# Kernel tuning notes

Measured on AMD Instinct MI355X. Metric: run time of the kernel, lower is better.

Reference implementation:

```python
import jax, jax.numpy as jnp
import numpy as np

B, S, C, H = 2, 3144, 256, 8
HD = C // H                      # head_dim = key_dim = 32
SCALE = HD ** -0.5
QN = 8                           # queriesNum hard-coded in source
KS = 5                           # lepe depthwise conv kernel


def setup_inputs() -> dict:
    key = jax.random.key(0)
    ks = jax.random.split(key, 10)
    gain_qkv = 2 ** (-2.5) * (2.0 / (C + C)) ** 0.5  # xavier_normal std with gain 2^-2.5
    gain_out = (2.0 / (C + C)) ** 0.5
    return {
        "x": jax.random.normal(ks[0], (B, S, C), jnp.float32),
        "mask": jax.random.uniform(ks[1], (B, S, S), jnp.float32),
        "wq": jax.random.normal(ks[2], (C, C), jnp.float32) * gain_qkv,
        "bq": jnp.zeros((C,), jnp.float32),
        "wk": jax.random.normal(ks[3], (C, C), jnp.float32) * gain_qkv,
        "bk": jnp.zeros((C,), jnp.float32),
        "wv": jax.random.normal(ks[4], (C, C), jnp.float32) * gain_qkv,
        "bv": jnp.zeros((C,), jnp.float32),
        "lepe_w": jax.random.normal(ks[5], (KS, KS, 1, C), jnp.float32) * 0.05,  # depthwise HWIO
        "lepe_b": jnp.zeros((C,), jnp.float32),
        "wo": jax.random.normal(ks[6], (C, C), jnp.float32) * gain_out,
        "bo": jnp.zeros((C,), jnp.float32),
        "h": 56,
        "w": 56,
    }


def _dwconv(x_nhwc, kern, bias):
    # depthwise 5x5, stride 1, padding 2 (groups = channels)
    y = jax.lax.conv_general_dilated(
        x_nhwc, kern, window_strides=(1, 1), padding=((2, 2), (2, 2)),
        dimension_numbers=("NHWC", "HWIO", "NHWC"),
        feature_group_count=x_nhwc.shape[-1])
    return y + bias


def reference(x, mask, wq, bq, wk, bk, wv, bv, lepe_w, lepe_b, wo, bo, h, w):
    b, s, c = x.shape
    q = x @ wq.T + bq
    k = (x @ wk.T + bk) * SCALE
    v = x @ wv.T + bv
    # lepe positional residual on the non-query tokens
    lepe = _dwconv(v[:, QN:].reshape(b, h, w, c), lepe_w, lepe_b).reshape(b, h * w, c)
    qh = q.reshape(b, s, H, HD).transpose(0, 2, 1, 3)   # (b, H, s, hd)
    kh = k.reshape(b, s, H, HD).transpose(0, 2, 1, 3)
    vh = kh  # faithful to source: v_h = k.reshape(...)  (scaled k used as values)
    qk = jnp.einsum("bhqd,bhkd->bhqk", qh, kh)
    qk = qk + jnp.log(mask[:, None] + 1e-6)              # isSoftMask=True path
    attn = jax.nn.softmax(qk, axis=-1)
    out = jnp.einsum("bhqk,bhkd->bhqd", attn, vh)
    out = out.transpose(0, 2, 1, 3).reshape(b, s, c)
    out = out.at[:, QN:].add(lepe)
    return out @ wo.T + bo
```

## Files before the change

### kernel.cpp

```cpp
#include <hip/hip_runtime.h>


#define S_LEN 3144
#define SP    3200
#define HEADS 8
#define HD    32
#define BATCH 2
#define MROWS (BATCH*S_LEN)
#define NPIX  3136
#define SCALE_F 0.17677669529663687f
#define KQ_SC   0.25504472665352026f

typedef __bf16 bf16x8  __attribute__((ext_vector_type(8)));
typedef __bf16 bf16x4  __attribute__((ext_vector_type(4)));
typedef float  floatx4 __attribute__((ext_vector_type(4)));
typedef short  shortx4 __attribute__((ext_vector_type(4)));
typedef _Float16 halfx4 __attribute__((ext_vector_type(4)));
typedef _Float16 halfx8 __attribute__((ext_vector_type(8)));

static __device__ __forceinline__ float bf2f(unsigned int h) {
  union { unsigned int u; float f; } v; v.u = h << 16; return v.f;
}
static __device__ __forceinline__ unsigned short f2bf(float f) {
  union { __bf16 b; unsigned short u; } v; v.b = (__bf16)f; return v.u;
}
static __device__ __forceinline__ bf16x8 ldcvt8(const float* __restrict__ p) {
  float4 a = *(const float4*)p;
  float4 b = *(const float4*)(p + 4);
  bf16x8 r;
  r[0]=(__bf16)a.x; r[1]=(__bf16)a.y; r[2]=(__bf16)a.z; r[3]=(__bf16)a.w;
  r[4]=(__bf16)b.x; r[5]=(__bf16)b.y; r[6]=(__bf16)b.z; r[7]=(__bf16)b.w;
  return r;
}

#define GLOBAL_AS __attribute__((address_space(1)))
#define LDS_AS    __attribute__((address_space(3)))
static __device__ __forceinline__ void gload_lds16(const void* g, void* l) {
  __builtin_amdgcn_global_load_lds((const GLOBAL_AS void*)g, (LDS_AS void*)l, 16, 0, 0);
}

#define FENCE4() asm volatile("s_waitcnt vmcnt(4)" ::: "memory")
#define FENCE2() asm volatile("s_waitcnt vmcnt(2)" ::: "memory")
#define FENCE0() asm volatile("s_waitcnt vmcnt(0)" ::: "memory")

__global__ __launch_bounds__(256) void k_prep(
    const float* __restrict__ x, const float* __restrict__ wq,
    const float* __restrict__ wk, const float* __restrict__ wv,
    unsigned short* __restrict__ xb, unsigned short* __restrict__ w3b,
    const float* __restrict__ mask, _Float16* __restrict__ pm)
{
  const int blk = blockIdx.x;
  if (blk < 882) {
    const int i = blk * 256 + threadIdx.x;
    const int NX = MROWS * 32;
    const int NW = 8192;
    const float* src;
    unsigned short* dst;
    if (i < NX) { src = x + (size_t)i * 8; dst = xb + (size_t)i * 8; }
    else {
      const int j = i - NX;
      if (j >= 3 * NW) return;
      src = (j < NW) ? wq + (size_t)j * 8
          : (j < 2 * NW) ? wk + (size_t)(j - NW) * 8
                         : wv + (size_t)(j - 2 * NW) * 8;
      dst = w3b + (size_t)j * 8;
    }
    bf16x8 v = ldcvt8(src);
    *(bf16x8*)dst = v;
    return;
  }
  const int mp = blk - 882;
  const int bs = mp % 400;
  const int by = mp / 400;
  const int b  = bs / 200, strip = bs % 200;
  const int t  = threadIdx.x;
  const int n  = t & 127;
  const int tsel = t >> 7;
  const int row = n >> 3;
  const int k2  = n & 7;
  const int g0  = (2 * k2) ^ (row & 15);
  const int gbase = g0 & ~1;
  const bool swp = (g0 & 1);

  int mr = strip * 16 + row; if (mr >= S_LEN) mr = S_LEN - 1;
  const float* src = mask + ((size_t)b * S_LEN + mr) * S_LEN;
  _Float16* dst0 = pm + ((size_t)bs * 50) * 1024 + n * 8;

#pragma unroll 1
  for (int tt = 0; tt < 5; ++tt) {
    const int tile = by * 10 + tt * 2 + tsel;
    const int c0 = tile * 64 + gbase * 4;
    float4 a = make_float4(-1e-6f, -1e-6f, -1e-6f, -1e-6f);
    float4 c = a;
    if (c0 < S_LEN) {
      a = *(const float4*)(src + c0);
      c = *(const float4*)(src + c0 + 4);
    }
    const float4 fst = swp ? c : a;
    const float4 snd = swp ? a : c;
    halfx8 o;
    o[0] = (_Float16)(fst.x + 1e-6f); o[1] = (_Float16)(fst.y + 1e-6f);
    o[2] = (_Float16)(fst.z + 1e-6f); o[3] = (_Float16)(fst.w + 1e-6f);
    o[4] = (_Float16)(snd.x + 1e-6f); o[5] = (_Float16)(snd.y + 1e-6f);
    o[6] = (_Float16)(snd.z + 1e-6f); o[7] = (_Float16)(snd.w + 1e-6f);
    *(halfx8*)(dst0 + (size_t)tile * 1024) = o;
  }
}

__global__ __launch_bounds__(256) void k_qkv(
    const unsigned short* __restrict__ xb, const unsigned short* __restrict__ w3b,
    const float* __restrict__ bqp, const float* __restrict__ bkp,
    const float* __restrict__ bvp,
    unsigned short* __restrict__ qws, unsigned short* __restrict__ kws,
    unsigned short* __restrict__ vfrag, unsigned short* __restrict__ vstage)
{
  __shared__ unsigned short lds_t[64 * 65];
  const int lane = threadIdx.x & 63;
  const int wid  = threadIdx.x >> 6;
  const int c    = lane & 15, quad = lane >> 4;
  const int bsel  = blockIdx.x / 50;
  const int stile = blockIdx.x % 50;
  const int srow0 = stile * 64;
  const int ncol = blockIdx.y * 64;
  const int wsel = ncol >> 8;
  const int col0 = ncol & 255;

  const float* bptr = (wsel == 0) ? bqp : (wsel == 1) ? bkp : bvp;

  const int srow = srow0 + wid * 16 + c;
  const int arow = bsel * S_LEN + ((srow < S_LEN) ? srow : 0);
  const unsigned short* ap = xb  + (size_t)arow * 256 + quad * 8;
  const unsigned short* bp = w3b + (size_t)(ncol + c) * 256 + quad * 8;

  floatx4 acc[4];
#pragma unroll
  for (int ct = 0; ct < 4; ++ct) acc[ct] = (floatx4){0.f, 0.f, 0.f, 0.f};

#pragma unroll
  for (int ks = 0; ks < 8; ++ks) {
    bf16x8 af = *(const bf16x8*)(ap + ks * 32);
#pragma unroll
    for (int ct = 0; ct < 4; ++ct) {
      bf16x8 bf = *(const bf16x8*)(bp + (size_t)ct * 16 * 256 + ks * 32);
      acc[ct] = __builtin_amdgcn_mfma_f32_16x16x32_bf16(af, bf, acc[ct], 0, 0, 0);
    }
  }

#pragma unroll
  for (int ct = 0; ct < 4; ++ct) {
    const int col = col0 + ct * 16 + c;
    const float bias = bptr[col];
#pragma unroll
    for (int r = 0; r < 4; ++r) {
      const int s = srow0 + wid * 16 + quad * 4 + r;
      const int valid = (s < S_LEN);
      const float v = acc[ct][r] + bias;
      if (wsel == 0) {
        qws[(((size_t)(bsel * HEADS + (col >> 5))) * SP + s) * HD + (col & 31)] =
            valid ? f2bf(v) : (unsigned short)0;
      } else if (wsel == 1) {
        kws[(((size_t)(bsel * HEADS + (col >> 5))) * SP + s) * HD + (col & 31)] =
            valid ? f2bf(v * KQ_SC) : (unsigned short)0;
        lds_t[(ct * 16 + c) * 65 + (wid * 16 + quad * 4 + r)] =
            valid ? f2bf(v * SCALE_F) : (unsigned short)0;
      } else {
        if (valid) vstage[(size_t)(bsel * S_LEN + s) * 256 + col] = f2bf(v);
      }
    }
  }

  if (wsel == 1) {
    __syncthreads();
    const int tid = threadIdx.x;
#pragma unroll
    for (int j = 0; j < 4; ++j) {
      const int grp  = j * 4 + (tid >> 6);
      const int l    = tid & 63;
      const int ct2  = grp & 3;
      const int half = (grp >> 2) & 1;
      const int hsel = grp >> 3;
      const int cc = l & 15, qq = l >> 4;
      const int cl = hsel * 32 + half * 16 + cc;
      const int rb = ct2 * 16 + qq * 4;
      union { shortx4 s4; unsigned short u[4]; } pk;
#pragma unroll
      for (int e = 0; e < 4; ++e) pk.u[e] = lds_t[cl * 65 + rb + e];
      const int hglob = (col0 >> 5) + hsel;
      const size_t off =
          ((((size_t)(bsel * HEADS + hglob) * 50 + stile) * 4 + ct2) * 2 + half) * 64 + l;
      *(shortx4*)(vfrag + off * 4) = pk.s4;
    }
  }
}

__global__ __launch_bounds__(256) void k_lepe(const unsigned short* __restrict__ vws,
                                              const float* __restrict__ cw,
                                              const float* __restrict__ cb,
                                              unsigned short* __restrict__ lepe)
{
  int idx = blockIdx.x * 256 + threadIdx.x;
  if (idx >= BATCH * NPIX * 32) return;
  const int cg = idx & 31;
  const int p  = (idx >> 5) % NPIX;
  const int b  = idx / (NPIX * 32);
  const int y  = p / 56, xx = p - y * 56;

  float acc[8];
  {
    float4 b0 = *(const float4*)(cb + cg * 8);
    float4 b1 = *(const float4*)(cb + cg * 8 + 4);
    acc[0]=b0.x; acc[1]=b0.y; acc[2]=b0.z; acc[3]=b0.w;
    acc[4]=b1.x; acc[5]=b1.y; acc[6]=b1.z; acc[7]=b1.w;
  }
#pragma unroll
  for (int dy = -2; dy <= 2; ++dy) {
    const int yy = y + dy;
    if ((unsigned)yy >= 56u) continue;
#pragma unroll
    for (int dx = -2; dx <= 2; ++dx) {
      const int xs = xx + dx;
      if ((unsigned)xs >= 56u) continue;
      uint4 vv = *(const uint4*)(vws + (size_t)(b * S_LEN + 8 + yy * 56 + xs) * 256 + cg * 8);
      const float* wp = cw + (size_t)((dy + 2) * 5 + (dx + 2)) * 256 + cg * 8;
      float4 w0 = *(const float4*)wp;
      float4 w1 = *(const float4*)(wp + 4);
      unsigned int va[4] = {vv.x, vv.y, vv.z, vv.w};
      acc[0] += bf2f(va[0] & 0xFFFFu) * w0.x;  acc[1] += bf2f(va[0] >> 16) * w0.y;
      acc[2] += bf2f(va[1] & 0xFFFFu) * w0.z;  acc[3] += bf2f(va[1] >> 16) * w0.w;
      acc[4] += bf2f(va[2] & 0xFFFFu) * w1.x;  acc[5] += bf2f(va[2] >> 16) * w1.y;
      acc[6] += bf2f(va[3] & 0xFFFFu) * w1.z;  acc[7] += bf2f(va[3] >> 16) * w1.w;
    }
  }
  unsigned int o[4];
#pragma unroll
  for (int j = 0; j < 4; ++j)
    o[j] = (unsigned int)f2bf(acc[2*j]) | ((unsigned int)f2bf(acc[2*j+1]) << 16);
  *((uint4*)(lepe + (size_t)(b * NPIX + p) * 256 + cg * 8)) = make_uint4(o[0], o[1], o[2], o[3]);
}

static __device__ __forceinline__ void proc_tile_pre(
    int t, const unsigned short* __restrict__ kb,
    const unsigned short* __restrict__ vb,
    const _Float16* __restrict__ mb,
    int c, int quad, int lane, const bf16x8 qf,
    floatx4& o0, floatx4& o1, float& l_run)
{
  const int k0 = t * 64;
  bf16x8 kf[4]; shortx4 v0[4], v1[4];
  const unsigned short* tb = vb + (size_t)t * 2048;
#pragma unroll
  for (int ct = 0; ct < 4; ++ct) {
    kf[ct] = *(const bf16x8*)(kb + (size_t)(k0 + ct * 16 + c) * HD + quad * 8);
    v0[ct] = *(const shortx4*)(tb + (ct * 2 + 0) * 256 + lane * 4);
    v1[ct] = *(const shortx4*)(tb + (ct * 2 + 1) * 256 + lane * 4);
  }
  floatx4 s[4];
#pragma unroll
  for (int ct = 0; ct < 4; ++ct)
    s[ct] = __builtin_amdgcn_mfma_f32_16x16x32_bf16(kf[ct], qf,
               (floatx4){0.f,0.f,0.f,0.f}, 0, 0, 0);
  float ls = 0.f;
  shortx4 pf[4];
#pragma unroll
  for (int ct = 0; ct < 4; ++ct) {
    const halfx4 mv = *(const halfx4*)(mb + c * 64 + (((ct * 4 + quad) ^ c) * 4));
    float pr[4];
    pr[0] = (float)mv[0] * __builtin_amdgcn_exp2f(s[ct][0]);
    pr[1] = (float)mv[1] * __builtin_amdgcn_exp2f(s[ct][1]);
    pr[2] = (float)mv[2] * __builtin_amdgcn_exp2f(s[ct][2]);
    pr[3] = (float)mv[3] * __builtin_amdgcn_exp2f(s[ct][3]);
    ls += (pr[0] + pr[1]) + (pr[2] + pr[3]);
    union { bf16x4 b4; shortx4 s4; } u;
    u.b4[0]=(__bf16)pr[0]; u.b4[1]=(__bf16)pr[1]; u.b4[2]=(__bf16)pr[2]; u.b4[3]=(__bf16)pr[3];
    pf[ct] = u.s4;
  }
  l_run += ls;
#pragma unroll
  for (int ct = 0; ct < 4; ++ct) {
    o0 = __builtin_amdgcn_mfma_f32_16x16x16bf16_1k(v0[ct], pf[ct], o0, 0, 0, 0);
    o1 = __builtin_amdgcn_mfma_f32_16x16x16bf16_1k(v1[ct], pf[ct], o1, 0, 0, 0);
  }
}

static __device__ __forceinline__ void stage_pre(
    const _Float16* __restrict__ mp_t, int lane, _Float16* dst)
{
#pragma unroll
  for (int i = 0; i < 2; ++i)
    gload_lds16(mp_t + i * 512 + lane * 8, dst + i * 512);
}

__global__ __launch_bounds__(256) void k_flash_pre(
    const unsigned short* __restrict__ qws,
    const unsigned short* __restrict__ kws,
    const unsigned short* __restrict__ vfrag,
    const _Float16* __restrict__ pmask,
    const unsigned short* __restrict__ lepe,
    unsigned short* __restrict__ attn)
{
  __shared__ __align__(16) float smem[4][1024];
  const int lane = threadIdx.x & 63;
  const int wid  = threadIdx.x >> 6;
  const int c    = lane & 15, quad = lane >> 4;
  const int u    = blockIdx.x;
  const int xcd  = u & 7;
  const int slot = u >> 3;
  const int h    = slot & 7;
  const int p    = (slot >> 3) * 8 + xcd;
  const int b    = p / 200;
  const int strip = p - b * 200;
  const int qrow = strip * 16 + c;
  const size_t bh = (size_t)(b * HEADS + h);

  const bf16x8 qf = *(const bf16x8*)(qws + (bh * SP + qrow) * HD + quad * 8);
  const unsigned short* kb = kws + bh * SP * HD;
  const unsigned short* vb = vfrag + bh * (size_t)(50 * 2048);
  const _Float16* mpb = pmask + (size_t)(b * 200 + strip) * (50 * 1024);
  _Float16* mt = (_Float16*)&smem[wid][0];

  float l_run = 0.f;
  floatx4 o0 = (floatx4){0.f,0.f,0.f,0.f};
  floatx4 o1 = (floatx4){0.f,0.f,0.f,0.f};

  const int tbase = wid * 12;
  const int nt = (wid < 2) ? 13 : 12;

  stage_pre(mpb + tbase * 1024, lane, mt);

  for (int it = 0; it < nt; ++it) {
    const int t = (it < 12) ? tbase + it : 48 + wid;
    if (it + 1 < nt) {
      const int tn = (it + 1 < 12) ? tbase + it + 1 : 48 + wid;
      stage_pre(mpb + tn * 1024, lane, mt + ((it + 1) & 1) * 1024);
      FENCE2();
    } else {
      FENCE0();
    }
    proc_tile_pre(t, kb, vb, mt + (it & 1) * 1024, c, quad, lane, qf, o0, o1, l_run);
  }

#pragma unroll
  for (int r = 0; r < 4; ++r) {
    smem[wid][lane * 9 + r]     = o0[r];
    smem[wid][lane * 9 + 4 + r] = o1[r];
  }
  smem[wid][lane * 9 + 8] = l_run;
  __syncthreads();

  if (wid == 0) {
#pragma unroll
    for (int w = 1; w < 4; ++w) {
#pragma unroll
      for (int r = 0; r < 4; ++r) {
        o0[r] += smem[w][lane * 9 + r];
        o1[r] += smem[w][lane * 9 + 4 + r];
      }
      l_run += smem[w][lane * 9 + 8];
    }
    l_run += __shfl_xor(l_run, 16);
    l_run += __shfl_xor(l_run, 32);
    const float rl = 1.f / l_run;

    if (qrow < S_LEN) {
      const size_t obase = ((size_t)b * S_LEN + qrow) * 256 + h * 32;
      const size_t lbase = (qrow >= 8) ? (((size_t)b * NPIX + (qrow - 8)) * 256 + h * 32) : 0;
#pragma unroll
      for (int mt2 = 0; mt2 < 2; ++mt2) {
        floatx4 ov = mt2 ? o1 : o0;
#pragma unroll
        for (int r = 0; r < 4; ++r) {
          const int d = mt2 * 16 + quad * 4 + r;
          float val = ov[r] * rl;
          if (qrow >= 8) val += bf2f(lepe[lbase + d]);
          attn[obase + d] = f2bf(val);
        }
      }
    }
  }
}

template<bool TAIL>
static __device__ __forceinline__ void proc_tile_fb(
    int t, const unsigned short* __restrict__ kb,
    const unsigned short* __restrict__ vb,
    const float* __restrict__ mb,
    int c, int quad, int lane, const bf16x8 qf,
    floatx4& o0, floatx4& o1, float& l_run)
{
  const int k0 = t * 64;
  bf16x8 kf[4]; shortx4 v0[4], v1[4];
  const unsigned short* tb = vb + (size_t)t * 2048;
#pragma unroll
  for (int ct = 0; ct < 4; ++ct) {
    kf[ct] = *(const bf16x8*)(kb + (size_t)(k0 + ct * 16 + c) * HD + quad * 8);
    v0[ct] = *(const shortx4*)(tb + (ct * 2 + 0) * 256 + lane * 4);
    v1[ct] = *(const shortx4*)(tb + (ct * 2 + 1) * 256 + lane * 4);
  }
  floatx4 s[4];
#pragma unroll
  for (int ct = 0; ct < 4; ++ct)
    s[ct] = __builtin_amdgcn_mfma_f32_16x16x32_bf16(kf[ct], qf,
               (floatx4){0.f,0.f,0.f,0.f}, 0, 0, 0);
  float ls = 0.f;
  shortx4 pf[4];
#pragma unroll
  for (int ct = 0; ct < 4; ++ct) {
    const float4 mv = *(const float4*)(mb + c * 64 + (((ct * 4 + quad) ^ c) * 4));
    float pr[4];
    pr[0] = (mv.x + 1e-6f) * __builtin_amdgcn_exp2f(s[ct][0]);
    pr[1] = (mv.y + 1e-6f) * __builtin_amdgcn_exp2f(s[ct][1]);
    pr[2] = (mv.z + 1e-6f) * __builtin_amdgcn_exp2f(s[ct][2]);
    pr[3] = (mv.w + 1e-6f) * __builtin_amdgcn_exp2f(s[ct][3]);
    if (TAIL) {
      const int kk = k0 + ct * 16 + quad * 4;
#pragma unroll
      for (int r = 0; r < 4; ++r) if (kk + r >= S_LEN) pr[r] = 0.f;
    }
    ls += (pr[0] + pr[1]) + (pr[2] + pr[3]);
    union { bf16x4 b4; shortx4 s4; } u;
    u.b4[0]=(__bf16)pr[0]; u.b4[1]=(__bf16)pr[1]; u.b4[2]=(__bf16)pr[2]; u.b4[3]=(__bf16)pr[3];
    pf[ct] = u.s4;
  }
  l_run += ls;
#pragma unroll
  for (int ct = 0; ct < 4; ++ct) {
    o0 = __builtin_amdgcn_mfma_f32_16x16x16bf16_1k(v0[ct], pf[ct], o0, 0, 0, 0);
    o1 = __builtin_amdgcn_mfma_f32_16x16x16bf16_1k(v1[ct], pf[ct], o1, 0, 0, 0);
  }
}

static __device__ __forceinline__ void stage_mask_fb(
    const float* const (&msrc)[4], const int (&goff4)[4], int k0, float* dst)
{
#pragma unroll
  for (int i = 0; i < 4; ++i)
    gload_lds16(msrc[i] + (k0 + goff4[i]), dst + i * 256);
}

static __device__ __forceinline__ void stage_mask_tail_fb(
    const float* const (&msrc)[4], const int (&goff4)[4], int k0, float* dst)
{
#pragma unroll
  for (int i = 0; i < 4; ++i) {
    int kk = k0 + goff4[i];
    if (kk > S_LEN - 4) kk = S_LEN - 4;
    gload_lds16(msrc[i] + kk, dst + i * 256);
  }
}

__global__ __launch_bounds__(512) void k_flash_fb(
    const unsigned short* __restrict__ qws,
    const unsigned short* __restrict__ kws,
    const unsigned short* __restrict__ vfrag,
    const float* __restrict__ mask,
    const unsigned short* __restrict__ lepe,
    unsigned short* __restrict__ attn)
{
  __shared__ __align__(16) float smem[8][2048];
  const int lane = threadIdx.x & 63;
  const int wid  = threadIdx.x >> 6;
  const int c    = lane & 15, quad = lane >> 4;
  const int u    = blockIdx.x;
  const int xcd  = u & 7;
  const int slot = u >> 3;
  const int h    = slot & 7;
  const int p    = (slot >> 3) * 8 + xcd;
  const int b    = p / 200;
  const int strip = p - b * 200;
  const int qrow = strip * 16 + c;
  const size_t bh = (size_t)(b * HEADS + h);

  const bf16x8 qf = *(const bf16x8*)(qws + (bh * SP + qrow) * HD + quad * 8);
  const unsigned short* kb = kws + bh * SP * HD;
  const unsigned short* vb = vfrag + bh * (size_t)(50 * 2048);
  float* mt = &smem[wid][0];

  const float* msrc[4];
  int goff4[4];
#pragma unroll
  for (int i = 0; i < 4; ++i) {
    const int rq = i * 4 + (lane >> 4);
    int mr = strip * 16 + rq; if (mr >= S_LEN) mr = S_LEN - 1;
    msrc[i] = mask + ((size_t)b * S_LEN + mr) * S_LEN;
    goff4[i] = ((lane & 15) ^ rq) * 4;
  }

  float l_run = 0.f;
  floatx4 o0 = (floatx4){0.f,0.f,0.f,0.f};
  floatx4 o1 = (floatx4){0.f,0.f,0.f,0.f};

  const int tbase = wid * 6;
  const int nt = (wid < 2) ? 7 : 6;

  stage_mask_fb(msrc, goff4, tbase * 64, mt);

  for (int it = 0; it < nt; ++it) {
    const int t = (it < 6) ? tbase + it : 48 + wid;
    if (it + 1 < nt) {
      const int tn = (it + 1 < 6) ? tbase + it + 1 : 48 + wid;
      float* dst = mt + ((it + 1) & 1) * 1024;
      if (tn == 49) stage_mask_tail_fb(msrc, goff4, 49 * 64, dst);
      else          stage_mask_fb(msrc, goff4, tn * 64, dst);
      FENCE4();
    } else {
      FENCE0();
    }
    const float* mb = mt + (it & 1) * 1024;
    if (wid == 1 && it == 6)
      proc_tile_fb<true >(t, kb, vb, mb, c, quad, lane, qf, o0, o1, l_run);
    else
      proc_tile_fb<false>(t, kb, vb, mb, c, quad, lane, qf, o0, o1, l_run);
  }

#pragma unroll
  for (int r = 0; r < 4; ++r) {
    smem[wid][lane * 9 + r]     = o0[r];
    smem[wid][lane * 9 + 4 + r] = o1[r];
  }
  smem[wid][lane * 9 + 8] = l_run;
  __syncthreads();

  if (wid == 0) {
#pragma unroll
    for (int w = 1; w < 8; ++w) {
#pragma unroll
      for (int r = 0; r < 4; ++r) {
        o0[r] += smem[w][lane * 9 + r];
        o1[r] += smem[w][lane * 9 + 4 + r];
      }
      l_run += smem[w][lane * 9 + 8];
    }
    l_run += __shfl_xor(l_run, 16);
    l_run += __shfl_xor(l_run, 32);
    const float rl = 1.f / l_run;

    if (qrow < S_LEN) {
      const size_t obase = ((size_t)b * S_LEN + qrow) * 256 + h * 32;
      const size_t lbase = (qrow >= 8) ? (((size_t)b * NPIX + (qrow - 8)) * 256 + h * 32) : 0;
#pragma unroll
      for (int mt2 = 0; mt2 < 2; ++mt2) {
        floatx4 ov = mt2 ? o1 : o0;
#pragma unroll
        for (int r = 0; r < 4; ++r) {
          const int d = mt2 * 16 + quad * 4 + r;
          float val = ov[r] * rl;
          if (qrow >= 8) val += bf2f(lepe[lbase + d]);
          attn[obase + d] = f2bf(val);
        }
      }
    }
  }
}

__global__ __launch_bounds__(256) void k_oproj(
    const unsigned short* __restrict__ attn,
    const float* __restrict__ wop,
    const float* __restrict__ bop,
    float* __restrict__ out)
{
  const int lane = threadIdx.x & 63;
  const int wid  = threadIdx.x >> 6;
  const int c = lane & 15, quad = lane >> 4;
  const int row0 = blockIdx.x * 64 + wid * 16;
  const int col0 = blockIdx.y * 32;

  int arow = row0 + c; if (arow >= MROWS) arow = 0;
  const unsigned short* ap = attn + (size_t)arow * 256 + quad * 8;
  const float* bp = wop + (size_t)(col0 + c) * 256 + quad * 8;

  floatx4 acc[2];
#pragma unroll
  for (int ct = 0; ct < 2; ++ct) acc[ct] = (floatx4){0.f,0.f,0.f,0.f};
#pragma unroll
  for (int ks = 0; ks < 8; ++ks) {
    bf16x8 af = *(const bf16x8*)(ap + ks * 32);
#pragma unroll
    for (int ct = 0; ct < 2; ++ct) {
      bf16x8 bf = ldcvt8(bp + (size_t)ct * 16 * 256 + ks * 32);
      acc[ct] = __builtin_amdgcn_mfma_f32_16x16x32_bf16(af, bf, acc[ct], 0, 0, 0);
    }
  }
#pragma unroll
  for (int ct = 0; ct < 2; ++ct) {
    const int col = col0 + ct * 16 + c;
    const float bias = bop[col];
#pragma unroll
    for (int r = 0; r < 4; ++r) {
      const int row = row0 + quad * 4 + r;
      if (row >= MROWS) continue;
      out[(size_t)row * 256 + col] = acc[ct][r] + bias;
    }
  }
}

#define QW_OFF 0u
#define KW_OFF 3276800u
#define VF_OFF 6553600u
#define LE_OFF 9830400u
#define AT_OFF 13041664u
#define PM_OFF 16261120u
#define PM_NEED (16261120u + 40960000u)

extern "C" void kernel_launch(void* const* d_in, const int* in_sizes, int n_in,
                              void* d_out, int out_size, void* d_ws, size_t ws_size,
                              hipStream_t stream) {
  const float* x    = (const float*)d_in[0];
  const float* mask = (const float*)d_in[1];
  const float* wq   = (const float*)d_in[2];
  const float* bq   = (const float*)d_in[3];
  const float* wk   = (const float*)d_in[4];
  const float* bk   = (const float*)d_in[5];
  const float* wv   = (const float*)d_in[6];
  const float* bv   = (const float*)d_in[7];
  const float* lw   = (const float*)d_in[8];
  const float* lb   = (const float*)d_in[9];
  const float* wo   = (const float*)d_in[10];
  const float* bo   = (const float*)d_in[11];

  char* ws = (char*)d_ws;
  unsigned short* qws = (unsigned short*)(ws + QW_OFF);
  unsigned short* kws = (unsigned short*)(ws + KW_OFF);
  unsigned short* vfr = (unsigned short*)(ws + VF_OFF);
  unsigned short* w3b = (unsigned short*)(ws + LE_OFF);
  unsigned short* lpe = (unsigned short*)(ws + LE_OFF);
  unsigned short* atb = (unsigned short*)(ws + AT_OFF);
  unsigned short* vst = (unsigned short*)d_out;
  unsigned short* xb  = (unsigned short*)d_out + 1609728;
  float*          outf = (float*)d_out;

  const bool use_pre = (ws_size >= (size_t)PM_NEED);

  if (use_pre) {
    _Float16* pm = (_Float16*)(ws + PM_OFF);
    k_prep<<<2882, 256, 0, stream>>>(x, wq, wk, wv, xb, w3b, mask, pm);
    k_qkv<<<dim3(100, 12), 256, 0, stream>>>(xb, w3b, bq, bk, bv, qws, kws, vfr, vst);
    k_lepe<<<784, 256, 0, stream>>>(vst, lw, lb, lpe);
    k_flash_pre<<<3200, 256, 0, stream>>>(qws, kws, vfr, pm, lpe, atb);
  } else {
    k_prep<<<882, 256, 0, stream>>>(x, wq, wk, wv, xb, w3b, mask, (_Float16*)nullptr);
    k_qkv<<<dim3(100, 12), 256, 0, stream>>>(xb, w3b, bq, bk, bv, qws, kws, vfr, vst);
    k_lepe<<<784, 256, 0, stream>>>(vst, lw, lb, lpe);
    k_flash_fb<<<3200, 512, 0, stream>>>(qws, kws, vfr, mask, lpe, atb);
  }
  k_oproj<<<dim3(99, 8), 256, 0, stream>>>(atb, wo, bo, outf);
}
```

Measured before the change: 301.8 us.

## Rebalance kernel stages: mask prep with QKV, lepe with flash, add lepe in oproj

```diff
diff --git a/kernel.cpp b/kernel.cpp
--- a/kernel.cpp
+++ b/kernel.cpp
@@ -43,85 +43,89 @@
 #define FENCE2() asm volatile("s_waitcnt vmcnt(2)" ::: "memory")
 #define FENCE0() asm volatile("s_waitcnt vmcnt(0)" ::: "memory")
 
-__global__ __launch_bounds__(256) void k_prep(
+__global__ __launch_bounds__(256) void k_cvt(
     const float* __restrict__ x, const float* __restrict__ wq,
     const float* __restrict__ wk, const float* __restrict__ wv,
-    unsigned short* __restrict__ xb, unsigned short* __restrict__ w3b,
-    const float* __restrict__ mask, _Float16* __restrict__ pm)
-{
-  const int blk = blockIdx.x;
-  if (blk < 882) {
-    const int i = blk * 256 + threadIdx.x;
-    const int NX = MROWS * 32;
-    const int NW = 8192;
-    const float* src;
-    unsigned short* dst;
-    if (i < NX) { src = x + (size_t)i * 8; dst = xb + (size_t)i * 8; }
-    else {
-      const int j = i - NX;
-      if (j >= 3 * NW) return;
-      src = (j < NW) ? wq + (size_t)j * 8
-          : (j < 2 * NW) ? wk + (size_t)(j - NW) * 8
-                         : wv + (size_t)(j - 2 * NW) * 8;
-      dst = w3b + (size_t)j * 8;
-    }
-    bf16x8 v = ldcvt8(src);
-    *(bf16x8*)dst = v;
-    return;
-  }
-  const int mp = blk - 882;
-  const int bs = mp % 400;
-  const int by = mp / 400;
-  const int b  = bs / 200, strip = bs % 200;
-  const int t  = threadIdx.x;
-  const int n  = t & 127;
-  const int tsel = t >> 7;
-  const int row = n >> 3;
-  const int k2  = n & 7;
-  const int g0  = (2 * k2) ^ (row & 15);
-  const int gbase = g0 & ~1;
-  const bool swp = (g0 & 1);
-
-  int mr = strip * 16 + row; if (mr >= S_LEN) mr = S_LEN - 1;
-  const float* src = mask + ((size_t)b * S_LEN + mr) * S_LEN;
-  _Float16* dst0 = pm + ((size_t)bs * 50) * 1024 + n * 8;
-
-#pragma unroll 1
-  for (int tt = 0; tt < 5; ++tt) {
-    const int tile = by * 10 + tt * 2 + tsel;
-    const int c0 = tile * 64 + gbase * 4;
-    float4 a = make_float4(-1e-6f, -1e-6f, -1e-6f, -1e-6f);
-    float4 c = a;
-    if (c0 < S_LEN) {
-      a = *(const float4*)(src + c0);
-      c = *(const float4*)(src + c0 + 4);
-    }
-    const float4 fst = swp ? c : a;
-    const float4 snd = swp ? a : c;
-    halfx8 o;
-    o[0] = (_Float16)(fst.x + 1e-6f); o[1] = (_Float16)(fst.y + 1e-6f);
-    o[2] = (_Float16)(fst.z + 1e-6f); o[3] = (_Float16)(fst.w + 1e-6f);
-    o[4] = (_Float16)(snd.x + 1e-6f); o[5] = (_Float16)(snd.y + 1e-6f);
-    o[6] = (_Float16)(snd.z + 1e-6f); o[7] = (_Float16)(snd.w + 1e-6f);
-    *(halfx8*)(dst0 + (size_t)tile * 1024) = o;
-  }
-}
-
-__global__ __launch_bounds__(256) void k_qkv(
+    unsigned short* __restrict__ xb, unsigned short* __restrict__ w3b)
+{
+  const int i = blockIdx.x * 256 + threadIdx.x;
+  const int NX = MROWS * 32;
+  const int NW = 8192;
+  const float* src;
+  unsigned short* dst;
+  if (i < NX) { src = x + (size_t)i * 8; dst = xb + (size_t)i * 8; }
+  else {
+    const int j = i - NX;
+    if (j >= 3 * NW) return;
+    src = (j < NW) ? wq + (size_t)j * 8
+        : (j < 2 * NW) ? wk + (size_t)(j - NW) * 8
+                       : wv + (size_t)(j - 2 * NW) * 8;
+    dst = w3b + (size_t)j * 8;
+  }
+  bf16x8 v = ldcvt8(src);
+  *(bf16x8*)dst = v;
+}
+
+__global__ __launch_bounds__(256) void k_qkv_mp(
     const unsigned short* __restrict__ xb, const unsigned short* __restrict__ w3b,
     const float* __restrict__ bqp, const float* __restrict__ bkp,
     const float* __restrict__ bvp,
     unsigned short* __restrict__ qws, unsigned short* __restrict__ kws,
-    unsigned short* __restrict__ vfrag, unsigned short* __restrict__ vstage)
+    unsigned short* __restrict__ vfrag, unsigned short* __restrict__ vstage,
+    const float* __restrict__ mask, _Float16* __restrict__ pm)
 {
   __shared__ unsigned short lds_t[64 * 65];
+  const int blk = blockIdx.x;
+
+  if (blk >= 1200) {
+    const int mp = blk - 1200;
+    const int bs = mp % 400;
+    const int by = mp / 400;
+    const int b  = bs / 200, strip = bs % 200;
+    const int t  = threadIdx.x;
+    const int n  = t & 127;
+    const int tsel = t >> 7;
+    const int row = n >> 3;
+    const int k2  = n & 7;
+    const int g0  = (2 * k2) ^ (row & 15);
+    const int gbase = g0 & ~1;
+    const bool swp = (g0 & 1);
+
+    int mr = strip * 16 + row; if (mr >= S_LEN) mr = S_LEN - 1;
+    const float* src = mask + ((size_t)b * S_LEN + mr) * S_LEN;
+    _Float16* dst0 = pm + ((size_t)bs * 50) * 1024 + n * 8;
+
+#pragma unroll 1
+    for (int tt = 0; tt < 5; ++tt) {
+      const int tile = by * 10 + tt * 2 + tsel;
+      const int c0 = tile * 64 + gbase * 4;
+      float4 a = make_float4(-1e-6f, -1e-6f, -1e-6f, -1e-6f);
+      float4 c = a;
+      if (c0 < S_LEN) {
+        a = *(const float4*)(src + c0);
+        c = *(const float4*)(src + c0 + 4);
+      }
+      const float4 fst = swp ? c : a;
+      const float4 snd = swp ? a : c;
+      halfx8 o;
+      o[0] = (_Float16)(fst.x + 1e-6f); o[1] = (_Float16)(fst.y + 1e-6f);
+      o[2] = (_Float16)(fst.z + 1e-6f); o[3] = (_Float16)(fst.w + 1e-6f);
+      o[4] = (_Float16)(snd.x + 1e-6f); o[5] = (_Float16)(snd.y + 1e-6f);
+      o[6] = (_Float16)(snd.z + 1e-6f); o[7] = (_Float16)(snd.w + 1e-6f);
+      *(halfx8*)(dst0 + (size_t)tile * 1024) = o;
+    }
+    return;
+  }
+
+  const int xi = blk % 100;
+  const int yi = blk / 100;
   const int lane = threadIdx.x & 63;
   const int wid  = threadIdx.x >> 6;
   const int c    = lane & 15, quad = lane >> 4;
-  const int bsel  = blockIdx.x / 50;
-  const int stile = blockIdx.x % 50;
+  const int bsel  = xi / 50;
+  const int stile = xi % 50;
   const int srow0 = stile * 64;
-  const int ncol = blockIdx.y * 64;
+  const int ncol = yi * 64;
   const int wsel = ncol >> 8;
   const int col0 = ncol & 255;
 
@@ -193,12 +197,12 @@
   }
 }
 
-__global__ __launch_bounds__(256) void k_lepe(const unsigned short* __restrict__ vws,
-                                              const float* __restrict__ cw,
-                                              const float* __restrict__ cb,
-                                              unsigned short* __restrict__ lepe)
-{
-  int idx = blockIdx.x * 256 + threadIdx.x;
+static __device__ void lepe_block(int idx,
+                                  const unsigned short* __restrict__ vws,
+                                  const float* __restrict__ cw,
+                                  const float* __restrict__ cb,
+                                  unsigned short* __restrict__ lepe)
+{
   if (idx >= BATCH * NPIX * 32) return;
   const int cg = idx & 31;
   const int p  = (idx >> 5) % NPIX;
@@ -290,15 +294,21 @@
     gload_lds16(mp_t + i * 512 + lane * 8, dst + i * 512);
 }
 
-__global__ __launch_bounds__(256) void k_flash_pre(
+__global__ __launch_bounds__(256) void k_flash_lepe(
     const unsigned short* __restrict__ qws,
     const unsigned short* __restrict__ kws,
     const unsigned short* __restrict__ vfrag,
     const _Float16* __restrict__ pmask,
-    const unsigned short* __restrict__ lepe,
-    unsigned short* __restrict__ attn)
+    const unsigned short* __restrict__ vws,
+    const float* __restrict__ cw, const float* __restrict__ cb,
+    unsigned short* __restrict__ lepe_out,
+    float* __restrict__ atbf)
 {
   __shared__ __align__(16) float smem[4][1024];
+  if (blockIdx.x >= 3200) {
+    lepe_block((blockIdx.x - 3200) * 256 + threadIdx.x, vws, cw, cb, lepe_out);
+    return;
+  }
   const int lane = threadIdx.x & 63;
   const int wid  = threadIdx.x >> 6;
   const int c    = lane & 15, quad = lane >> 4;
@@ -362,21 +372,79 @@
     const float rl = 1.f / l_run;
 
     if (qrow < S_LEN) {
-      const size_t obase = ((size_t)b * S_LEN + qrow) * 256 + h * 32;
-      const size_t lbase = (qrow >= 8) ? (((size_t)b * NPIX + (qrow - 8)) * 256 + h * 32) : 0;
-#pragma unroll
-      for (int mt2 = 0; mt2 < 2; ++mt2) {
-        floatx4 ov = mt2 ? o1 : o0;
-#pragma unroll
-        for (int r = 0; r < 4; ++r) {
-          const int d = mt2 * 16 + quad * 4 + r;
-          float val = ov[r] * rl;
-          if (qrow >= 8) val += bf2f(lepe[lbase + d]);
-          attn[obase + d] = f2bf(val);
-        }
-      }
-    }
-  }
+      float* op = atbf + ((size_t)b * S_LEN + qrow) * 256 + h * 32;
+      float4 s0 = make_float4(o0[0]*rl, o0[1]*rl, o0[2]*rl, o0[3]*rl);
+      float4 s1 = make_float4(o1[0]*rl, o1[1]*rl, o1[2]*rl, o1[3]*rl);
+      *(float4*)(op + quad * 4)      = s0;
+      *(float4*)(op + 16 + quad * 4) = s1;
+    }
+  }
+}
+
+__global__ __launch_bounds__(256) void k_oproj(
+    const float* __restrict__ atbf,
+    const unsigned short* __restrict__ lepe,
+    const float* __restrict__ wop,
+    const float* __restrict__ bop,
+    float* __restrict__ out)
+{
+  const int lane = threadIdx.x & 63;
+  const int wid  = threadIdx.x >> 6;
+  const int c = lane & 15, quad = lane >> 4;
+  const int row0 = blockIdx.x * 64 + wid * 16;
+  const int col0 = blockIdx.y * 32;
+
+  int arow = row0 + c; if (arow >= MROWS) arow = 0;
+  const int bb = (arow >= S_LEN) ? 1 : 0;
+  const int sr = arow - bb * S_LEN;
+  const bool hasl = (sr >= 8);
+  const float* ap = atbf + (size_t)arow * 256 + quad * 8;
+  const unsigned short* lp =
+      lepe + (hasl ? (((size_t)bb * NPIX + (sr - 8)) * 256 + quad * 8) : 0);
+  const float* bp = wop + (size_t)(col0 + c) * 256 + quad * 8;
+
+  floatx4 acc[2];
+#pragma unroll
+  for (int ct = 0; ct < 2; ++ct) acc[ct] = (floatx4){0.f,0.f,0.f,0.f};
+#pragma unroll
+  for (int ks = 0; ks < 8; ++ks) {
+    float4 a0 = *(const float4*)(ap + ks * 32);
+    float4 a1 = *(const float4*)(ap + ks * 32 + 4);
+    if (hasl) {
+      uint4 lv = *(const uint4*)(lp + ks * 32);
+      a0.x += bf2f(lv.x & 0xFFFFu); a0.y += bf2f(lv.x >> 16);
+      a0.z += bf2f(lv.y & 0xFFFFu); a0.w += bf2f(lv.y >> 16);
+      a1.x += bf2f(lv.z & 0xFFFFu); a1.y += bf2f(lv.z >> 16);
+      a1.z += bf2f(lv.w & 0xFFFFu); a1.w += bf2f(lv.w >> 16);
+    }
+    bf16x8 af;
+    af[0]=(__bf16)a0.x; af[1]=(__bf16)a0.y; af[2]=(__bf16)a0.z; af[3]=(__bf16)a0.w;
+    af[4]=(__bf16)a1.x; af[5]=(__bf16)a1.y; af[6]=(__bf16)a1.z; af[7]=(__bf16)a1.w;
+#pragma unroll
+    for (int ct = 0; ct < 2; ++ct) {
+      bf16x8 bf = ldcvt8(bp + (size_t)ct * 16 * 256 + ks * 32);
+      acc[ct] = __builtin_amdgcn_mfma_f32_16x16x32_bf16(af, bf, acc[ct], 0, 0, 0);
+    }
+  }
+#pragma unroll
+  for (int ct = 0; ct < 2; ++ct) {
+    const int col = col0 + ct * 16 + c;
+    const float bias = bop[col];
+#pragma unroll
+    for (int r = 0; r < 4; ++r) {
+      const int row = row0 + quad * 4 + r;
+      if (row >= MROWS) continue;
+      out[(size_t)row * 256 + col] = acc[ct][r] + bias;
+    }
+  }
+}
+
+__global__ __launch_bounds__(256) void k_lepe_sa(const unsigned short* __restrict__ vws,
+                                                 const float* __restrict__ cw,
+                                                 const float* __restrict__ cb,
+                                                 unsigned short* __restrict__ lepe)
+{
+  lepe_block(blockIdx.x * 256 + threadIdx.x, vws, cw, cb, lepe);
 }
 
 template<bool TAIL>
@@ -453,8 +521,7 @@
     const unsigned short* __restrict__ kws,
     const unsigned short* __restrict__ vfrag,
     const float* __restrict__ mask,
-    const unsigned short* __restrict__ lepe,
-    unsigned short* __restrict__ attn)
+    float* __restrict__ atbf)
 {
   __shared__ __align__(16) float smem[8][2048];
   const int lane = threadIdx.x & 63;
@@ -535,60 +602,11 @@
     const float rl = 1.f / l_run;
 
     if (qrow < S_LEN) {
-      const size_t obase = ((size_t)b * S_LEN + qrow) * 256 + h * 32;
-      const size_t lbase = (qrow >= 8) ? (((size_t)b * NPIX + (qrow - 8)) * 256 + h * 32) : 0;
-#pragma unroll
-      for (int mt2 = 0; mt2 < 2; ++mt2) {
-        floatx4 ov = mt2 ? o1 : o0;
-#pragma unroll
-        for (int r = 0; r < 4; ++r) {
-          const int d = mt2 * 16 + quad * 4 + r;
-          float val = ov[r] * rl;
-          if (qrow >= 8) val += bf2f(lepe[lbase + d]);
-          attn[obase + d] = f2bf(val);
-        }
-      }
-    }
-  }
-}
-
-__global__ __launch_bounds__(256) void k_oproj(
-    const unsigned short* __restrict__ attn,
-    const float* __restrict__ wop,
-    const float* __restrict__ bop,
-    float* __restrict__ out)
-{
-  const int lane = threadIdx.x & 63;
-  const int wid  = threadIdx.x >> 6;
-  const int c = lane & 15, quad = lane >> 4;
-  const int row0 = blockIdx.x * 64 + wid * 16;
-  const int col0 = blockIdx.y * 32;
-
-  int arow = row0 + c; if (arow >= MROWS) arow = 0;
-  const unsigned short* ap = attn + (size_t)arow * 256 + quad * 8;
-  const float* bp = wop + (size_t)(col0 + c) * 256 + quad * 8;
-
-  floatx4 acc[2];
-#pragma unroll
-  for (int ct = 0; ct < 2; ++ct) acc[ct] = (floatx4){0.f,0.f,0.f,0.f};
-#pragma unroll
-  for (int ks = 0; ks < 8; ++ks) {
-    bf16x8 af = *(const bf16x8*)(ap + ks * 32);
-#pragma unroll
-    for (int ct = 0; ct < 2; ++ct) {
-      bf16x8 bf = ldcvt8(bp + (size_t)ct * 16 * 256 + ks * 32);
-      acc[ct] = __builtin_amdgcn_mfma_f32_16x16x32_bf16(af, bf, acc[ct], 0, 0, 0);
-    }
-  }
-#pragma unroll
-  for (int ct = 0; ct < 2; ++ct) {
-    const int col = col0 + ct * 16 + c;
-    const float bias = bop[col];
-#pragma unroll
-    for (int r = 0; r < 4; ++r) {
-      const int row = row0 + quad * 4 + r;
-      if (row >= MROWS) continue;
-      out[(size_t)row * 256 + col] = acc[ct][r] + bias;
+      float* op = atbf + ((size_t)b * S_LEN + qrow) * 256 + h * 32;
+      float4 s0 = make_float4(o0[0]*rl, o0[1]*rl, o0[2]*rl, o0[3]*rl);
+      float4 s1 = make_float4(o1[0]*rl, o1[1]*rl, o1[2]*rl, o1[3]*rl);
+      *(float4*)(op + quad * 4)      = s0;
+      *(float4*)(op + 16 + quad * 4) = s1;
     }
   }
 }
@@ -598,8 +616,8 @@
 #define VF_OFF 6553600u
 #define LE_OFF 9830400u
 #define AT_OFF 13041664u
-#define PM_OFF 16261120u
-#define PM_NEED (16261120u + 40960000u)
+#define PM_OFF 19480576u
+#define PM_NEED (19480576u + 40960000u)
 
 extern "C" void kernel_launch(void* const* d_in, const int* in_sizes, int n_in,
                               void* d_out, int out_size, void* d_ws, size_t ws_size,
@@ -623,24 +641,23 @@
   unsigned short* vfr = (unsigned short*)(ws + VF_OFF);
   unsigned short* w3b = (unsigned short*)(ws + LE_OFF);
   unsigned short* lpe = (unsigned short*)(ws + LE_OFF);
-  unsigned short* atb = (unsigned short*)(ws + AT_OFF);
+  float*          atf = (float*)(ws + AT_OFF);
   unsigned short* vst = (unsigned short*)d_out;
   unsigned short* xb  = (unsigned short*)d_out + 1609728;
   float*          outf = (float*)d_out;
 
   const bool use_pre = (ws_size >= (size_t)PM_NEED);
 
+  k_cvt<<<882, 256, 0, stream>>>(x, wq, wk, wv, xb, w3b);
   if (use_pre) {
     _Float16* pm = (_Float16*)(ws + PM_OFF);
-    k_prep<<<2882, 256, 0, stream>>>(x, wq, wk, wv, xb, w3b, mask, pm);
-    k_qkv<<<dim3(100, 12), 256, 0, stream>>>(xb, w3b, bq, bk, bv, qws, kws, vfr, vst);
-    k_lepe<<<784, 256, 0, stream>>>(vst, lw, lb, lpe);
-    k_flash_pre<<<3200, 256, 0, stream>>>(qws, kws, vfr, pm, lpe, atb);
+    k_qkv_mp<<<3200, 256, 0, stream>>>(xb, w3b, bq, bk, bv, qws, kws, vfr, vst, mask, pm);
+    k_flash_lepe<<<3984, 256, 0, stream>>>(qws, kws, vfr, pm, vst, lw, lb, lpe, atf);
   } else {
-    k_prep<<<882, 256, 0, stream>>>(x, wq, wk, wv, xb, w3b, mask, (_Float16*)nullptr);
-    k_qkv<<<dim3(100, 12), 256, 0, stream>>>(xb, w3b, bq, bk, bv, qws, kws, vfr, vst);
-    k_lepe<<<784, 256, 0, stream>>>(vst, lw, lb, lpe);
-    k_flash_fb<<<3200, 512, 0, stream>>>(qws, kws, vfr, mask, lpe, atb);
-  }
-  k_oproj<<<dim3(99, 8), 256, 0, stream>>>(atb, wo, bo, outf);
-}
+    k_qkv_mp<<<1200, 256, 0, stream>>>(xb, w3b, bq, bk, bv, qws, kws, vfr, vst,
+                                       mask, (_Float16*)nullptr);
+    k_lepe_sa<<<784, 256, 0, stream>>>(vst, lw, lb, lpe);
+    k_flash_fb<<<3200, 512, 0, stream>>>(qws, kws, vfr, mask, atf);
+  }
+  k_oproj<<<dim3(99, 8), 256, 0, stream>>>(atf, lpe, wo, bo, outf);
+}
```

Result: faster. 295.8 us (-2.0%).
